# Kernel tuning notes

Hardware: AMD Instinct MI355X
Metric: run time of the kernel (lower is better)

## Reference

```python
import jax, jax.numpy as jnp
import numpy as np

KERNEL_MUL = 2.0
KERNEL_NUM = 5


def _mmd_channel(s, t):
    """Multi-bandwidth Gaussian-kernel MMD for one channel. s,t: [B, D]."""
    B = s.shape[0]
    total = jnp.concatenate([s, t], axis=0)            # [2B, D]
    sq = jnp.sum(total * total, axis=1)                # [2B]
    # ||xi - xj||^2 via Gram identity (avoids [2B,2B,D] intermediate)
    L2 = sq[:, None] + sq[None, :] - 2.0 * (total @ total.T)  # [2B, 2B]
    n = 2 * B
    # torch uses L2_distance.data -> bandwidth is detached
    bandwidth = jax.lax.stop_gradient(jnp.sum(L2)) / (n * n - n)
    bandwidth = bandwidth / (KERNEL_MUL ** (KERNEL_NUM // 2))
    bws = bandwidth * (KERNEL_MUL ** jnp.arange(KERNEL_NUM, dtype=s.dtype))  # [K_num]
    kernels = jnp.sum(jnp.exp(-L2[None, :, :] / bws[:, None, None]), axis=0)  # [2B, 2B]
    XX = kernels[:B, :B]
    YY = kernels[B:, B:]
    XY = kernels[:B, B:]
    YX = kernels[B:, :B]
    return jnp.mean(XX + YY - XY - YX)


def setup_inputs() -> dict:
    key = jax.random.key(0)
    k1, k2 = jax.random.split(key)
    B, K, H, W = 128, 21, 64, 64
    source = jax.random.normal(k1, (B, K, H, W), dtype=jnp.float32)
    target = jax.random.normal(k2, (B, K, H, W), dtype=jnp.float32)
    return {"source": source, "target": target}


def reference(source, target):
    B, K = source.shape[0], source.shape[1]
    s = source.reshape(B, K, -1)  # [B, K, D]
    t = target.reshape(B, K, -1)
    per_channel = jax.vmap(_mmd_channel, in_axes=(1, 1))(s, t)  # [K]
    return jnp.sum(per_channel) / K
```

## Files before the change

kernel.cpp:

```cpp
#include <hip/hip_runtime.h>
#include <hip/hip_bf16.h>
#include <stdint.h>

typedef __attribute__((ext_vector_type(4))) float f32x4;
typedef __attribute__((ext_vector_type(8))) short bf16x8;

#define NCH 21
#define NROW 256
#define DIM 4096
#define BK 64
#define NTILE 10

__device__ const int g_TI[NTILE] = {0, 0, 0, 0, 1, 1, 1, 2, 2, 3};
__device__ const int g_TJ[NTILE] = {0, 1, 2, 3, 1, 2, 3, 2, 3, 3};

__device__ __forceinline__ uint32_t pack_bf2(float x, float y) {
  __hip_bfloat162 h = __float22bfloat162_rn(float2{x, y});
  union { __hip_bfloat162 h; uint32_t u; } c;
  c.h = h;
  return c.u;
}

__global__ __launch_bounds__(1024, 4) void gram_kernel(
    const float* __restrict__ src, const float* __restrict__ tgt,
    float* __restrict__ Gp, int kshift, int kchunk) {
  const int P = 1 << kshift;
  const int g = blockIdx.x;
  const int ch = g >> kshift;
  const int ks = g & (P - 1);
  const int kbase = ks * kchunk;
  const int tid = threadIdx.x;
  const int lane = tid & 63;
  const int wave = tid >> 6;

  __shared__ __attribute__((aligned(16))) ushort S[256 * 64];

  f32x4 acc[4][4];
#pragma unroll
  for (int m = 0; m < 4; ++m)
#pragma unroll
    for (int n = 0; n < 4; ++n)
      acc[m][n] = (f32x4){0.f, 0.f, 0.f, 0.f};

  const float* gptr[4];
  int lw[4];
#pragma unroll
  for (int i = 0; i < 4; ++i) {
    const int id = i * 1024 + tid;
    const int row = id >> 4;
    const int c16 = id & 15;
    const float* base = (row < 128) ? src + ((size_t)row * NCH + ch) * DIM
                                    : tgt + ((size_t)(row - 128) * NCH + ch) * DIM;
    gptr[i] = base + kbase + c16 * 4;
    const int sch = (c16 >> 1) ^ (row & 7);
    lw[i] = row * 64 + sch * 8 + (c16 & 1) * 4;
  }

  const int ti = g_TI[wave < NTILE ? wave : 0];
  const int tj = g_TJ[wave < NTILE ? wave : 0];

  const int nk = kchunk / BK;

  f32x4 v[4];
#pragma unroll
  for (int i = 0; i < 4; ++i) v[i] = *reinterpret_cast<const f32x4*>(gptr[i]);

  for (int it = 0; it < nk; ++it) {
    __syncthreads();
#pragma unroll
    for (int i = 0; i < 4; ++i) {
      uint2 wv;
      wv.x = pack_bf2(v[i].x, v[i].y);
      wv.y = pack_bf2(v[i].z, v[i].w);
      *reinterpret_cast<uint2*>(&S[lw[i]]) = wv;
    }
    if (it + 1 < nk) {
      const int ko = (it + 1) * BK;
#pragma unroll
      for (int i = 0; i < 4; ++i)
        v[i] = *reinterpret_cast<const f32x4*>(gptr[i] + ko);
    }
    asm volatile("s_waitcnt lgkmcnt(0)" ::: "memory");
    __builtin_amdgcn_s_barrier();
    asm volatile("" ::: "memory");

    if (wave < NTILE) {
#pragma unroll
      for (int kk = 0; kk < 2; ++kk) {
        const int chunk = kk * 4 + (lane >> 4);
        bf16x8 a[4], b[4];
#pragma unroll
        for (int m = 0; m < 4; ++m) {
          const int row = ti * 64 + m * 16 + (lane & 15);
          a[m] = *reinterpret_cast<const bf16x8*>(
              &S[row * 64 + (chunk ^ (row & 7)) * 8]);
        }
#pragma unroll
        for (int n = 0; n < 4; ++n) {
          const int row = tj * 64 + n * 16 + (lane & 15);
          b[n] = *reinterpret_cast<const bf16x8*>(
              &S[row * 64 + (chunk ^ (row & 7)) * 8]);
        }
#pragma unroll
        for (int m = 0; m < 4; ++m)
#pragma unroll
          for (int n = 0; n < 4; ++n)
            acc[m][n] = __builtin_amdgcn_mfma_f32_16x16x32_bf16(a[m], b[n],
                                                                acc[m][n], 0, 0, 0);
      }
    }
  }

  if (wave < NTILE) {
    float* gp = Gp + (size_t)(ch * P + ks) * (NROW * NROW);
#pragma unroll
    for (int m = 0; m < 4; ++m)
#pragma unroll
      for (int n = 0; n < 4; ++n) {
        const int grow = ti * 64 + m * 16 + ((lane >> 4) << 2);
        const int gcol = tj * 64 + n * 16 + (lane & 15);
#pragma unroll
        for (int j = 0; j < 4; ++j)
          gp[(size_t)(grow + j) * NROW + gcol] = acc[m][n][j];
      }
  }
}

__device__ __forceinline__ float block_sum256(float v, float* sm) {
#pragma unroll
  for (int o = 32; o > 0; o >>= 1) v += __shfl_down(v, o, 64);
  const int lane = threadIdx.x & 63;
  const int wv = threadIdx.x >> 6;
  if (lane == 0) sm[wv] = v;
  __syncthreads();
  float r = 0.f;
  if (threadIdx.x == 0) r = sm[0] + sm[1] + sm[2] + sm[3];
  __syncthreads();
  return r;
}

__global__ __launch_bounds__(256) void foldsum_kernel(
    const f32x4* __restrict__ Gp, f32x4* __restrict__ Gf,
    float* __restrict__ sums, int P) {
  const int t = blockIdx.x;
  const int ch = blockIdx.y;
  const int ti = g_TI[t], tj = g_TJ[t];
  const bool isdiag = (ti == tj);
  const int tid = threadIdx.x;
  float s = 0.f, tr = 0.f;
#pragma unroll
  for (int i = 0; i < 4; ++i) {
    const int idx4 = tid * 4 + i;
    const int rrow = idx4 >> 4;
    const int c4 = idx4 & 15;
    const int base_v = (ti * 64 + rrow) * 64 + tj * 16 + c4;
    f32x4 v = Gp[(size_t)(ch * P) * 16384 + base_v];
    for (int p = 1; p < P; ++p) v += Gp[(size_t)(ch * P + p) * 16384 + base_v];
    Gf[(size_t)ch * 16384 + base_v] = v;
    s += (v.x + v.y) + (v.z + v.w);
    if (isdiag) {
      const int cb = c4 * 4;
#pragma unroll
      for (int e = 0; e < 4; ++e)
        if (cb + e == rrow) tr += v[e];
    }
  }
  __shared__ float sm[4];
  float sG = block_sum256(s, sm);
  float sT = block_sum256(tr, sm);
  if (tid == 0) {
    sums[ch * 20 + t] = sG;
    if (isdiag) sums[ch * 20 + 10 + ti] = sT;
  }
}

__global__ __launch_bounds__(256) void mmd_kernel(const float* __restrict__ Gf,
                                                  const float* __restrict__ sums,
                                                  float* __restrict__ partial) {
  const int t = blockIdx.x;
  const int ch = blockIdx.y;
  const int ti = g_TI[t], tj = g_TJ[t];
  const int tid = threadIdx.x;
  const float* gg = Gf + (size_t)ch * (NROW * NROW);

  const float* sc = sums + ch * 20;
  float sumG = 0.f;
#pragma unroll
  for (int k = 0; k < NTILE; ++k)
    sumG += (g_TI[k] == g_TJ[k] ? 1.f : 2.f) * sc[k];
  const float trace = (sc[10] + sc[11]) + (sc[12] + sc[13]);
  const float sumL2 = 2.f * NROW * trace - 2.f * sumG;
  const float bw = sumL2 / (float)(NROW * NROW - NROW) * 0.25f;
  float inv[5];
#pragma unroll
  for (int a = 0; a < 5; ++a) inv[a] = -1.f / (bw * (float)(1 << a));

  __shared__ float dA[64], dB[64];
  if (tid < 64) dA[tid] = gg[(size_t)(ti * 64 + tid) * (NROW + 1)];
  else if (tid < 128) dB[tid - 64] = gg[(size_t)(tj * 64 + (tid - 64)) * (NROW + 1)];
  __syncthreads();

  const int col = tid & 63;
  const int qq = tid >> 6;
  const float dj = dB[col];
  float acc = 0.f;
#pragma unroll 4
  for (int it = 0; it < 16; ++it) {
    const int r = it * 4 + qq;
    const float L2 = dA[r] + dj - 2.f * gg[(size_t)(ti * 64 + r) * NROW + tj * 64 + col];
    float kv = 0.f;
#pragma unroll
    for (int a = 0; a < 5; ++a) kv += __expf(L2 * inv[a]);
    acc += kv;
  }
  __shared__ float sm[4];
  float tot = block_sum256(acc, sm);
  if (tid == 0) {
    float wgt = (ti == tj) ? 1.f : 2.f;
    float sgn = ((ti >= 2) == (tj >= 2)) ? 1.f : -1.f;
    partial[ch * NTILE + t] = tot * wgt * sgn;
  }
}

__global__ __launch_bounds__(256) void final_kernel(const float* __restrict__ partial,
                                                    float* __restrict__ out) {
  const int tid = threadIdx.x;
  float v = (tid < NCH * NTILE) ? partial[tid] : 0.f;
  __shared__ float sm[4];
  float tot = block_sum256(v, sm);
  if (tid == 0) out[0] = tot * (1.f / (NCH * 128.f * 128.f));
}

extern "C" void kernel_launch(void* const* d_in, const int* in_sizes, int n_in,
                              void* d_out, int out_size, void* d_ws, size_t ws_size,
                              hipStream_t stream) {
  const float* src = (const float*)d_in[0];
  const float* tgt = (const float*)d_in[1];
  float* out = (float*)d_out;
  const size_t GSZ = (size_t)NROW * NROW;

  int kshift = 0;
  if (ws_size >= (NCH * 9 * GSZ + 512) * sizeof(float)) kshift = 3;
  else if (ws_size >= (NCH * 5 * GSZ + 512) * sizeof(float)) kshift = 2;
  else if (ws_size >= (NCH * 3 * GSZ + 512) * sizeof(float)) kshift = 1;
  const int P = 1 << kshift;

  float* Gp = (float*)d_ws;
  float* Gf = (P > 1) ? Gp + (size_t)NCH * P * GSZ : Gp;
  float* sums = Gf + (size_t)NCH * GSZ;
  float* partial = sums + NCH * 20;

  gram_kernel<<<dim3(NCH * P), 1024, 0, stream>>>(src, tgt, Gp, kshift,
                                                  DIM >> kshift);
  foldsum_kernel<<<dim3(NTILE, NCH), 256, 0, stream>>>((const f32x4*)Gp,
                                                       (f32x4*)Gf, sums, P);
  mmd_kernel<<<dim3(NTILE, NCH), 256, 0, stream>>>(Gf, sums, partial);
  final_kernel<<<1, 256, 0, stream>>>(partial, out);
}
```

Measured before the change: 44.15 us.

## Widen gram K-tile to 256 and stage loads per row with interleaved prefetch

Raises the K-slice held in shared memory from 64 to 256 bf16 columns, so the 256-row LDS tile grows to 128KB and the loop runs a quarter as many barrier-separated iterations. Global loads are re-mapped so each wave reads whole contiguous row segments (64 lanes × 4 floats), staged in four groups that alternate with LDS stores, with only the first group prefetched across the barrier. The aim is to cut synchronisation overhead and improve load coalescing. In exchange, LDS use limits occupancy to one block per CU and less of the global-load latency overlaps with MFMA work.

```diff
diff --git a/kernel.cpp b/kernel.cpp
--- a/kernel.cpp
+++ b/kernel.cpp
@@ -8,7 +8,7 @@
 #define NCH 21
 #define NROW 256
 #define DIM 4096
-#define BK 64
+#define BK 256
 #define NTILE 10
 
 __device__ const int g_TI[NTILE] = {0, 0, 0, 0, 1, 1, 1, 2, 2, 3};
@@ -33,7 +33,7 @@
   const int lane = tid & 63;
   const int wave = tid >> 6;
 
-  __shared__ __attribute__((aligned(16))) ushort S[256 * 64];
+  __shared__ __attribute__((aligned(16))) ushort S[256 * 256];
 
   f32x4 acc[4][4];
 #pragma unroll
@@ -42,64 +42,69 @@
     for (int n = 0; n < 4; ++n)
       acc[m][n] = (f32x4){0.f, 0.f, 0.f, 0.f};
 
-  const float* gptr[4];
-  int lw[4];
-#pragma unroll
-  for (int i = 0; i < 4; ++i) {
-    const int id = i * 1024 + tid;
-    const int row = id >> 4;
-    const int c16 = id & 15;
-    const float* base = (row < 128) ? src + ((size_t)row * NCH + ch) * DIM
-                                    : tgt + ((size_t)(row - 128) * NCH + ch) * DIM;
-    gptr[i] = base + kbase + c16 * 4;
-    const int sch = (c16 >> 1) ^ (row & 7);
-    lw[i] = row * 64 + sch * 8 + (c16 & 1) * 4;
-  }
-
-  const int ti = g_TI[wave < NTILE ? wave : 0];
-  const int tj = g_TJ[wave < NTILE ? wave : 0];
+  const float* p0 = src + ((size_t)wave * NCH + ch) * DIM + kbase + lane * 4;
+  const float* p1 = tgt + ((size_t)wave * NCH + ch) * DIM + kbase + lane * 4;
+  const size_t rs = (size_t)16 * NCH * DIM;
+  const int lw_base = wave * 256 + (((lane >> 1) ^ (wave & 7)) << 3) + (lane & 1) * 4;
+
+#define LD(i, ko) (*reinterpret_cast<const f32x4*>( \
+    ((i) < 8 ? p0 + (size_t)(i) * rs : p1 + (size_t)((i) - 8) * rs) + (ko)))
+#define ST(vv, i)                                          \
+  {                                                        \
+    uint2 wv;                                              \
+    wv.x = pack_bf2((vv).x, (vv).y);                       \
+    wv.y = pack_bf2((vv).z, (vv).w);                       \
+    *reinterpret_cast<uint2*>(&S[lw_base + (i) * 4096]) = wv; \
+  }
 
   const int nk = kchunk / BK;
 
-  f32x4 v[4];
-#pragma unroll
-  for (int i = 0; i < 4; ++i) v[i] = *reinterpret_cast<const f32x4*>(gptr[i]);
+  f32x4 vA[4], vB[4];
+#pragma unroll
+  for (int j = 0; j < 4; ++j) vA[j] = LD(j, 0);
 
   for (int it = 0; it < nk; ++it) {
+    const int ko = it * BK;
     __syncthreads();
 #pragma unroll
-    for (int i = 0; i < 4; ++i) {
-      uint2 wv;
-      wv.x = pack_bf2(v[i].x, v[i].y);
-      wv.y = pack_bf2(v[i].z, v[i].w);
-      *reinterpret_cast<uint2*>(&S[lw[i]]) = wv;
-    }
+    for (int j = 0; j < 4; ++j) vB[j] = LD(4 + j, ko);
+#pragma unroll
+    for (int j = 0; j < 4; ++j) ST(vA[j], 0 + j);
+#pragma unroll
+    for (int j = 0; j < 4; ++j) vA[j] = LD(8 + j, ko);
+#pragma unroll
+    for (int j = 0; j < 4; ++j) ST(vB[j], 4 + j);
+#pragma unroll
+    for (int j = 0; j < 4; ++j) vB[j] = LD(12 + j, ko);
+#pragma unroll
+    for (int j = 0; j < 4; ++j) ST(vA[j], 8 + j);
+#pragma unroll
+    for (int j = 0; j < 4; ++j) ST(vB[j], 12 + j);
     if (it + 1 < nk) {
-      const int ko = (it + 1) * BK;
-#pragma unroll
-      for (int i = 0; i < 4; ++i)
-        v[i] = *reinterpret_cast<const f32x4*>(gptr[i] + ko);
+#pragma unroll
+      for (int j = 0; j < 4; ++j) vA[j] = LD(j, ko + BK);
     }
     asm volatile("s_waitcnt lgkmcnt(0)" ::: "memory");
     __builtin_amdgcn_s_barrier();
     asm volatile("" ::: "memory");
 
     if (wave < NTILE) {
-#pragma unroll
-      for (int kk = 0; kk < 2; ++kk) {
+      const int ti = g_TI[wave], tj = g_TJ[wave];
+#pragma unroll
+      for (int kk = 0; kk < 8; ++kk) {
         const int chunk = kk * 4 + (lane >> 4);
         bf16x8 a[4], b[4];
 #pragma unroll
         for (int m = 0; m < 4; ++m) {
           const int row = ti * 64 + m * 16 + (lane & 15);
           a[m] = *reinterpret_cast<const bf16x8*>(
-              &S[row * 64 + (chunk ^ (row & 7)) * 8]);
+              &S[row * 256 + ((chunk ^ (row & 7)) << 3)]);
         }
 #pragma unroll
         for (int n = 0; n < 4; ++n) {
           const int row = tj * 64 + n * 16 + (lane & 15);
           b[n] = *reinterpret_cast<const bf16x8*>(
-              &S[row * 64 + (chunk ^ (row & 7)) * 8]);
+              &S[row * 256 + ((chunk ^ (row & 7)) << 3)]);
         }
 #pragma unroll
         for (int m = 0; m < 4; ++m)
@@ -112,6 +117,7 @@
   }
 
   if (wave < NTILE) {
+    const int ti = g_TI[wave], tj = g_TJ[wave];
     float* gp = Gp + (size_t)(ch * P + ks) * (NROW * NROW);
 #pragma unroll
     for (int m = 0; m < 4; ++m)
@@ -124,6 +130,8 @@
           gp[(size_t)(grow + j) * NROW + gcol] = acc[m][n][j];
       }
   }
+#undef LD
+#undef ST
 }
 
 __device__ __forceinline__ float block_sum256(float v, float* sm) {
```

Result: slower. 52.87 us (+19.7%).
